# Optimization experiments

Measured on AMD Instinct MI355X. Metric: run time of the kernel, lower is better.

The kernel has to match this reference:

```python
import jax, jax.numpy as jnp
import numpy as np

B, S, E = 2, 2048, 1024
H = 16
HD = E // H           # 64
KD = 64               # k_dim
VD = 64               # v_dim
SCALE = 1.0 / np.float32(np.sqrt(KD))


def setup_inputs() -> dict:
    key = jax.random.key(0)
    ks = jax.random.split(key, 10)
    return {
        "x": jax.random.normal(ks[0], (B, S, E), dtype=jnp.float32),
        "mask": jax.random.uniform(ks[1], (S, S), dtype=jnp.float32),
        "Wq": jax.random.normal(ks[2], (HD, KD), dtype=jnp.float32) * 0.05,
        "bq": jax.random.normal(ks[3], (KD,), dtype=jnp.float32) * 0.05,
        "Wk": jax.random.normal(ks[4], (HD, KD), dtype=jnp.float32) * 0.05,
        "bk": jax.random.normal(ks[5], (KD,), dtype=jnp.float32) * 0.05,
        "Wv": jax.random.normal(ks[6], (HD, VD), dtype=jnp.float32) * 0.05,
        "bv": jax.random.normal(ks[7], (VD,), dtype=jnp.float32) * 0.05,
        "Wo": jax.random.normal(ks[8], (H * VD, E), dtype=jnp.float32) * 0.05,
        "bo": jax.random.normal(ks[9], (E,), dtype=jnp.float32) * 0.05,
    }


def reference(x, mask, Wq, bq, Wk, bk, Wv, bv, Wo, bo):
    b, s, e = x.shape
    # (B, S, E) -> (B, H, S, head_dim)
    xh = x.reshape(b, s, H, HD).transpose(0, 2, 1, 3)
    q = jnp.einsum('bhsd,dk->bhsk', xh, Wq) + bq   # (B,H,S,KD)
    k = jnp.einsum('bhsd,dk->bhsk', xh, Wk) + bk   # (B,H,S,KD)
    v = jnp.einsum('bhsd,dv->bhsv', xh, Wv) + bv   # (B,H,S,VD)
    sim = jnp.einsum('bhqk,bhsk->bhqs', q, k) * SCALE  # (B,H,S,S)
    sim = sim * mask[None, None, :, :]                  # multiplicative mask
    attn = jax.nn.softmax(sim, axis=-1)
    out = jnp.einsum('bhqs,bhsv->bhqv', attn, v)        # (B,H,S,VD)
    out = out.transpose(0, 2, 1, 3).reshape(b, s, H * VD)
    return out @ Wo + bo
```

## Files before the change

kernel.cpp:

```cpp
#include <hip/hip_runtime.h>
#include <hip/hip_bf16.h>

#define SS 2048
#define EE 1024
#define SCALE 0.125f
#define LOG2E 1.44269504088896f

typedef __attribute__((ext_vector_type(8))) short short8;
typedef __attribute__((ext_vector_type(4))) float float4v;
typedef __attribute__((ext_vector_type(4))) unsigned int uint4v;

__device__ __forceinline__ unsigned short f2bf(float f) {
  unsigned int u = __float_as_uint(f);
  unsigned int lsb = (u >> 16) & 1u;
  u += 0x7fffu + lsb;
  return (unsigned short)(u >> 16);
}
__device__ __forceinline__ unsigned int pk2bf(float a, float b) {
  __hip_bfloat162 h = __float22bfloat162_rn(float2{a, b});
  return *reinterpret_cast<unsigned int*>(&h);
}

__global__ __launch_bounds__(256) void fused_qkv(
    const float* __restrict__ x,
    const float* __restrict__ Wq, const float* __restrict__ Wk,
    const float* __restrict__ Wv,
    const float* __restrict__ bq, const float* __restrict__ bk,
    const float* __restrict__ bv,
    const float* __restrict__ mask, const float* __restrict__ Wo,
    unsigned short* __restrict__ Q, unsigned short* __restrict__ Kp,
    unsigned short* __restrict__ Vf,
    unsigned short* __restrict__ maskP, unsigned short* __restrict__ WoT)
{
  __shared__ __align__(16) unsigned short w3t[192 * 72];
  __shared__ __align__(16) unsigned short xt[64 * 72];
  __shared__ __align__(16) unsigned short ob[12288];
  __shared__ float sBias[192];
  __shared__ unsigned short t[64 * 65];
  int blk = blockIdx.x;
  int tid = threadIdx.x;

  if (blk >= 512) {
    if (blk < 2560) {
      int idx = (blk - 512) * 256 + tid;
      int lane = idx & 63, step = (idx >> 6) & 63, qt = idx >> 12;
      int li = lane & 15, g = lane >> 4;
      const float c = SCALE * LOG2E;
      const float* mrow = mask + (size_t)(qt * 16 + li) * SS + step * 32 + g * 4;
      float4 a = *(const float4*)mrow;
      float4 bb = *(const float4*)(mrow + 16);
      uint4v o;
      o.x = pk2bf(a.x * c, a.y * c);
      o.y = pk2bf(a.z * c, a.w * c);
      o.z = pk2bf(bb.x * c, bb.y * c);
      o.w = pk2bf(bb.z * c, bb.w * c);
      *(uint4v*)(maskP + (size_t)idx * 8) = o;
      return;
    }
    int wblk = blk - 2560;
    int k0 = (wblk >> 4) * 64, n0 = (wblk & 15) * 64;
#pragma unroll
    for (int i = 0; i < 16; ++i) {
      int e = tid + i * 256; int kk = e >> 6, nn = e & 63;
      t[nn * 65 + kk] = f2bf(Wo[(size_t)(k0 + kk) * 1024 + n0 + nn]);
    }
    __syncthreads();
#pragma unroll
    for (int i = 0; i < 16; ++i) {
      int e = tid + i * 256; int nn = e >> 6, kk = e & 63;
      WoT[(size_t)(n0 + nn) * 1024 + k0 + kk] = t[nn * 65 + kk];
    }
    return;
  }

  int bh = blk >> 4;
  int s0blk = (blk & 15) * 128;
  int b = bh >> 4, h = bh & 15;
  int wv = tid >> 6, lane = tid & 63;
  int li = lane & 15, g = lane >> 4;

  {
    const float* Ws[3] = {Wq, Wk, Wv};
#pragma unroll
    for (int m = 0; m < 3; ++m) {
      const float* W = Ws[m];
#pragma unroll
      for (int i = 0; i < 16; ++i) {
        int e = tid + i * 256; int d = e >> 6, n = e & 63;
        w3t[(m * 64 + n) * 72 + d] = f2bf(W[e]);
      }
    }
  }
  if (tid < 192) sBias[tid] = (tid < 64) ? bq[tid] : (tid < 128 ? bk[tid - 64] : bv[tid - 128]);

  for (int half = 0; half < 2; ++half) {
    int s0 = s0blk + half * 64;
    if (half) __syncthreads();
    const float* xbase = x + ((size_t)(b * SS + s0)) * EE + h * 64;
#pragma unroll
    for (int it = 0; it < 4; ++it) {
      int flat = tid + it * 256;
      int row = flat >> 4, ch = flat & 15;
      float4 v = *(const float4*)(xbase + (size_t)row * EE + ch * 4);
      uint2 u; u.x = pk2bf(v.x, v.y); u.y = pk2bf(v.z, v.w);
      *(uint2*)(xt + row * 72 + ch * 4) = u;
    }
    __syncthreads();

    int mrow = wv * 16;
    short8 af[2];
#pragma unroll
    for (int ks = 0; ks < 2; ++ks)
      af[ks] = *(const short8*)(xt + (mrow + li) * 72 + ks * 32 + g * 8);

    float4v acc[12];
#pragma unroll
    for (int i = 0; i < 12; ++i) acc[i] = (float4v){0, 0, 0, 0};
#pragma unroll
    for (int ks = 0; ks < 2; ++ks)
#pragma unroll
      for (int nb = 0; nb < 12; ++nb) {
        short8 bfr = *(const short8*)(w3t + (nb * 16 + li) * 72 + ks * 32 + g * 8);
        acc[nb] = __builtin_amdgcn_mfma_f32_16x16x32_bf16(af[ks], bfr, acc[nb], 0, 0, 0);
      }

#pragma unroll
    for (int nb = 0; nb < 12; ++nb) {
      float bias = sBias[nb * 16 + li];
      int mtx = nb >> 2, sub = nb & 3;
#pragma unroll
      for (int r = 0; r < 4; ++r) {
        unsigned short v = f2bf(acc[nb][r] + bias);
        int sl = mrow + g * 4 + r;
        int stp = sl >> 5, s5 = sl & 31;
        if (mtx == 0) {
          ob[sl * 64 + sub * 16 + li] = v;
        } else if (mtx == 1) {
          int sb = s5 >> 4, lik = s5 & 15;
          int part = sub >> 1;
          int gk = ((sub & 1) << 1) | (li >> 3);
          ob[4096 + stp * 2048 + (sb * 2 + part) * 512 + (gk * 16 + lik) * 8 + (li & 7)] = v;
        } else {
          int pos = ((s5 >> 2) & 3) * 8 + ((s5 >> 4) & 1) * 4 + (s5 & 3);
          ob[8192 + stp * 2048 + sub * 512 + ((pos >> 3) * 16 + li) * 8 + (pos & 7)] = v;
        }
      }
    }
    __syncthreads();

    unsigned short* Qg = Q + ((size_t)bh * SS + s0) * 64;
    unsigned short* Kg = Kp + (size_t)bh * 131072 + (s0 >> 5) * 2048;
    unsigned short* Vg = Vf + (size_t)bh * 131072 + (s0 >> 5) * 2048;
#pragma unroll
    for (int i = 0; i < 6; ++i) {
      int slot = tid + i * 256;
      int rgn = slot >> 9, off = (slot & 511) * 8;
      short8 v = *(const short8*)(ob + rgn * 4096 + off);
      unsigned short* dst = (rgn == 0) ? (Qg + off) : (rgn == 1 ? (Kg + off) : (Vg + off));
      *(short8*)dst = v;
    }
  }
}

__global__ __launch_bounds__(256) void attn_kernel(
    const unsigned short* __restrict__ Q, const unsigned short* __restrict__ Kp,
    const unsigned short* __restrict__ Vf, const unsigned short* __restrict__ maskP,
    unsigned short* __restrict__ AO)
{
  __shared__ __align__(16) unsigned short tr_all[4 * 32 * 72];
  int tid = threadIdx.x, wv = tid >> 6, lane = tid & 63;
  int li = lane & 15, g = lane >> 4;
  int virt = (blockIdx.x & 7) * 64 + (blockIdx.x >> 3);
  int wave_id = virt * 4 + wv;
  int bh = wave_id >> 6;
  int q0 = (wave_id & 63) * 32;

  short8 qf[2][2];
#pragma unroll
  for (int t = 0; t < 2; ++t) {
    const unsigned short* Qb = Q + ((size_t)bh * SS + q0 + t * 16 + li) * 64;
    qf[t][0] = *(const short8*)(Qb + g * 8);
    qf[t][1] = *(const short8*)(Qb + 32 + g * 8);
  }

  const unsigned short* Kg = Kp + (size_t)bh * 131072 + lane * 8;
  const unsigned short* Vg = Vf + (size_t)bh * 131072 + lane * 8;
  const unsigned short* Mg0 = maskP + (size_t)(q0 >> 4) * 32768 + lane * 8;
  const unsigned short* Mg1 = Mg0 + 32768;

  unsigned short ov = (li == 0) ? (unsigned short)0x3F80 : (unsigned short)0;
  short8 vones = {(short)ov, (short)ov, (short)ov, (short)ov,
                  (short)ov, (short)ov, (short)ov, (short)ov};

  float4v acc[2][4];
#pragma unroll
  for (int t = 0; t < 2; ++t)
#pragma unroll
    for (int nb = 0; nb < 4; ++nb) acc[t][nb] = (float4v){0, 0, 0, 0};
  float4v accd[2] = {{0, 0, 0, 0}, {0, 0, 0, 0}};

  float4v st[2][2];

  short8 kA[4], kB[4], vA[4], vB[4];
  uint4v mA0, mA1, mB0, mB1;
  {
    short8 k0[4];
#pragma unroll
    for (int i = 0; i < 4; ++i) {
      k0[i] = *(const short8*)(Kg + i * 512);
      kA[i] = *(const short8*)(Kg + 2048 + i * 512);
      kB[i] = *(const short8*)(Kg + 2 * 2048 + i * 512);
      vA[i] = *(const short8*)(Vg + i * 512);
      vB[i] = *(const short8*)(Vg + 2048 + i * 512);
    }
    mA0 = *(const uint4v*)Mg0;
    mA1 = *(const uint4v*)Mg1;
    mB0 = *(const uint4v*)(Mg0 + 512);
    mB1 = *(const uint4v*)(Mg1 + 512);
#pragma unroll
    for (int t = 0; t < 2; ++t)
#pragma unroll
      for (int sb = 0; sb < 2; ++sb) {
        float4v s = {0, 0, 0, 0};
        s = __builtin_amdgcn_mfma_f32_16x16x32_bf16(k0[sb * 2], qf[t][0], s, 0, 0, 0);
        s = __builtin_amdgcn_mfma_f32_16x16x32_bf16(k0[sb * 2 + 1], qf[t][1], s, 0, 0, 0);
        st[t][sb] = s;
      }
  }

  const unsigned short* kpA = Kg + 3 * 2048;
  const unsigned short* kpB = Kg + 4 * 2048;
  const unsigned short* vpA = Vg + 2 * 2048;
  const unsigned short* vpB = Vg + 3 * 2048;
  const unsigned short* mp0 = Mg0 + 2 * 512;
  const unsigned short* mp1 = Mg1 + 2 * 512;

  auto half_step = [&](short8 (&kf)[4], short8 (&vf)[4], uint4v& m0c, uint4v& m1c,
                       const unsigned short* kre, const unsigned short* vre,
                       const unsigned short* mre0, const unsigned short* mre1) {
    short8 pf[2];
#pragma unroll
    for (int t = 0; t < 2; ++t) {
      uint4v pw2;
#pragma unroll
      for (int sb = 0; sb < 2; ++sb) {
#pragma unroll
        for (int hh = 0; hh < 2; ++hh) {
          unsigned int mm = (t == 0) ? m0c[sb * 2 + hh] : m1c[sb * 2 + hh];
          float p0 = __builtin_amdgcn_exp2f(st[t][sb][2 * hh] * __uint_as_float(mm << 16));
          float p1 = __builtin_amdgcn_exp2f(st[t][sb][2 * hh + 1] * __uint_as_float(mm & 0xffff0000u));
          pw2[sb * 2 + hh] = pk2bf(p0, p1);
        }
      }
      pf[t] = *(short8*)&pw2;
    }
    m0c = *(const uint4v*)mre0;
    m1c = *(const uint4v*)mre1;
    __builtin_amdgcn_s_setprio(1);
#pragma unroll
    for (int t = 0; t < 2; ++t)
#pragma unroll
      for (int sb = 0; sb < 2; ++sb) {
        float4v s = {0, 0, 0, 0};
        s = __builtin_amdgcn_mfma_f32_16x16x32_bf16(kf[sb * 2], qf[t][0], s, 0, 0, 0);
        s = __builtin_amdgcn_mfma_f32_16x16x32_bf16(kf[sb * 2 + 1], qf[t][1], s, 0, 0, 0);
        st[t][sb] = s;
      }
    __builtin_amdgcn_s_setprio(0);
#pragma unroll
    for (int i = 0; i < 4; ++i)
      kf[i] = *(const short8*)(kre + i * 512);
    __builtin_amdgcn_s_setprio(1);
#pragma unroll
    for (int nb = 0; nb < 4; ++nb) {
      acc[0][nb] = __builtin_amdgcn_mfma_f32_16x16x32_bf16(vf[nb], pf[0], acc[0][nb], 0, 0, 0);
      acc[1][nb] = __builtin_amdgcn_mfma_f32_16x16x32_bf16(vf[nb], pf[1], acc[1][nb], 0, 0, 0);
    }
    accd[0] = __builtin_amdgcn_mfma_f32_16x16x32_bf16(vones, pf[0], accd[0], 0, 0, 0);
    accd[1] = __builtin_amdgcn_mfma_f32_16x16x32_bf16(vones, pf[1], accd[1], 0, 0, 0);
    __builtin_amdgcn_s_setprio(0);
#pragma unroll
    for (int i = 0; i < 4; ++i)
      vf[i] = *(const short8*)(vre + i * 512);
  };

#pragma unroll 1
  for (int su = 0; su < 32; ++su) {
    half_step(kA, vA, mA0, mA1, kpA, vpA, mp0, mp1);
    half_step(kB, vB, mB0, mB1, kpB, vpB, mp0 + 512, mp1 + 512);
    kpA += 4096; kpB += 4096; vpA += 4096; vpB += 4096;
    mp0 += 1024; mp1 += 1024;
  }

  unsigned short* tr = tr_all + wv * (32 * 72);
#pragma unroll
  for (int t = 0; t < 2; ++t) {
    float den = __shfl(accd[t][0], li, 64);
    float rd = 1.0f / den;
#pragma unroll
    for (int nb = 0; nb < 4; ++nb) {
      int base = (t * 16 + li) * 72 + nb * 16 + g * 4;
      *(unsigned int*)(tr + base)     = pk2bf(acc[t][nb][0] * rd, acc[t][nb][1] * rd);
      *(unsigned int*)(tr + base + 2) = pk2bf(acc[t][nb][2] * rd, acc[t][nb][3] * rd);
    }
  }
  asm volatile("s_waitcnt lgkmcnt(0)" ::: "memory");

  int b = bh >> 4, h = bh & 15;
  int rrow = lane >> 3, part = lane & 7;
#pragma unroll
  for (int i = 0; i < 4; ++i) {
    int row = i * 8 + rrow;
    short8 o = *(const short8*)(tr + row * 72 + part * 8);
    *(short8*)(AO + ((size_t)(b * SS + q0 + row)) * EE + h * 64 + part * 8) = o;
  }
}

__global__ __launch_bounds__(256) void out_gemm(
    const unsigned short* __restrict__ AO, const unsigned short* __restrict__ WoT,
    const float* __restrict__ bo, float* __restrict__ out)
{
  __shared__ __align__(16) unsigned short at[128 * 72];
  __shared__ __align__(16) unsigned short bt[64 * 72];
  int tid = threadIdx.x, wv = tid >> 6, lane = tid & 63;
  int li = lane & 15, g = lane >> 4;
  int m0 = (blockIdx.x >> 4) * 128;
  int n0 = (blockIdx.x & 15) * 64;
  int wm = (wv & 1) * 64, wn = (wv >> 1) * 32;

  const unsigned short* Ag = AO + (size_t)m0 * 1024;
  const unsigned short* Bg = WoT + (size_t)n0 * 1024;
  int srow = tid >> 3, scol = (tid & 7) * 8;

  short8 apre[4], bpre[2];
  auto ldst = [&](int k0) {
#pragma unroll
    for (int i = 0; i < 4; ++i)
      apre[i] = *(const short8*)(Ag + (size_t)(srow + i * 32) * 1024 + k0 + scol);
#pragma unroll
    for (int i = 0; i < 2; ++i) {
      int slot = tid + i * 256;
      int row = slot >> 3, col = (slot & 7) * 8;
      bpre[i] = *(const short8*)(Bg + (size_t)row * 1024 + k0 + col);
    }
  };

  float4v acc[4][2];
#pragma unroll
  for (int mt = 0; mt < 4; ++mt)
#pragma unroll
    for (int nt = 0; nt < 2; ++nt) acc[mt][nt] = (float4v){0, 0, 0, 0};

  ldst(0);
  for (int k0 = 0; k0 < 1024; k0 += 64) {
    __syncthreads();
#pragma unroll
    for (int i = 0; i < 4; ++i)
      *(short8*)(at + (srow + i * 32) * 72 + scol) = apre[i];
#pragma unroll
    for (int i = 0; i < 2; ++i) {
      int slot = tid + i * 256;
      int row = slot >> 3, col = (slot & 7) * 8;
      *(short8*)(bt + row * 72 + col) = bpre[i];
    }
    int nk = (k0 + 64 < 1024) ? k0 + 64 : 0;
    ldst(nk);
    __syncthreads();
#pragma unroll
    for (int ks = 0; ks < 2; ++ks) {
      short8 afr[4], bfr[2];
#pragma unroll
      for (int mt = 0; mt < 4; ++mt)
        afr[mt] = *(const short8*)(at + (wm + mt * 16 + li) * 72 + ks * 32 + g * 8);
#pragma unroll
      for (int nt = 0; nt < 2; ++nt)
        bfr[nt] = *(const short8*)(bt + (wn + nt * 16 + li) * 72 + ks * 32 + g * 8);
#pragma unroll
      for (int mt = 0; mt < 4; ++mt)
#pragma unroll
        for (int nt = 0; nt < 2; ++nt)
          acc[mt][nt] = __builtin_amdgcn_mfma_f32_16x16x32_bf16(afr[mt], bfr[nt], acc[mt][nt], 0, 0, 0);
    }
  }
#pragma unroll
  for (int nt = 0; nt < 2; ++nt) {
    float bof = bo[n0 + wn + nt * 16 + li];
#pragma unroll
    for (int mt = 0; mt < 4; ++mt)
#pragma unroll
      for (int r = 0; r < 4; ++r)
        out[(size_t)(m0 + wm + mt * 16 + g * 4 + r) * 1024 + n0 + wn + nt * 16 + li] =
            acc[mt][nt][r] + bof;
  }
}

extern "C" void kernel_launch(void* const* d_in, const int* in_sizes, int n_in,
                              void* d_out, int out_size, void* d_ws, size_t ws_size,
                              hipStream_t stream) {
  const float* x    = (const float*)d_in[0];
  const float* mask = (const float*)d_in[1];
  const float* Wq   = (const float*)d_in[2];
  const float* bq   = (const float*)d_in[3];
  const float* Wk   = (const float*)d_in[4];
  const float* bk   = (const float*)d_in[5];
  const float* Wv   = (const float*)d_in[6];
  const float* bv   = (const float*)d_in[7];
  const float* Wo   = (const float*)d_in[8];
  const float* bo   = (const float*)d_in[9];
  float* out = (float*)d_out;

  unsigned short* ws = (unsigned short*)d_ws;
  unsigned short* Q     = ws;
  unsigned short* Kp    = ws + 4194304;
  unsigned short* Vf    = ws + 8388608;
  unsigned short* AO    = ws + 12582912;
  unsigned short* maskP = ws + 16777216;
  unsigned short* WoT   = ws + 20971520;

  fused_qkv<<<2816, 256, 0, stream>>>(x, Wq, Wk, Wv, bq, bk, bv, mask, Wo,
                                      Q, Kp, Vf, maskP, WoT);
  attn_kernel<<<512, 256, 0, stream>>>(Q, Kp, Vf, maskP, AO);
  out_gemm<<<512, 256, 0, stream>>>(AO, WoT, bo, out);
}
```

Measured before the change: 172.1 us.

## Load MFMA fragments directly from global memory in out_gemm, dropping LDS staging

The output projection GEMM no longer stages A and B tiles through shared memory with block barriers. Each wave now loads its MFMA operand fragments straight from global memory into registers, double-buffered two k-steps ahead. This removes LDS writes, LDS reads and syncthreads. In exchange, data shared between waves is no longer reused: each wave re-fetches rows that other waves also read, which raises global/L2 traffic and register use. The global reads are also less coalesced, since each lane reads 16-byte pieces at row strides.

```diff
diff --git a/kernel.cpp b/kernel.cpp
--- a/kernel.cpp
+++ b/kernel.cpp
@@ -320,30 +320,29 @@
     const unsigned short* __restrict__ AO, const unsigned short* __restrict__ WoT,
     const float* __restrict__ bo, float* __restrict__ out)
 {
-  __shared__ __align__(16) unsigned short at[128 * 72];
-  __shared__ __align__(16) unsigned short bt[64 * 72];
   int tid = threadIdx.x, wv = tid >> 6, lane = tid & 63;
   int li = lane & 15, g = lane >> 4;
   int m0 = (blockIdx.x >> 4) * 128;
   int n0 = (blockIdx.x & 15) * 64;
   int wm = (wv & 1) * 64, wn = (wv >> 1) * 32;
 
-  const unsigned short* Ag = AO + (size_t)m0 * 1024;
-  const unsigned short* Bg = WoT + (size_t)n0 * 1024;
-  int srow = tid >> 3, scol = (tid & 7) * 8;
-
-  short8 apre[4], bpre[2];
-  auto ldst = [&](int k0) {
-#pragma unroll
-    for (int i = 0; i < 4; ++i)
-      apre[i] = *(const short8*)(Ag + (size_t)(srow + i * 32) * 1024 + k0 + scol);
-#pragma unroll
-    for (int i = 0; i < 2; ++i) {
-      int slot = tid + i * 256;
-      int row = slot >> 3, col = (slot & 7) * 8;
-      bpre[i] = *(const short8*)(Bg + (size_t)row * 1024 + k0 + col);
-    }
+  const unsigned short* Abase = AO + (size_t)(m0 + wm + li) * 1024 + g * 8;
+  const unsigned short* Bbase = WoT + (size_t)(n0 + wn + li) * 1024 + g * 8;
+
+  auto ldA = [&](short8 (&A)[4][2], int k0) {
+#pragma unroll
+    for (int mt = 0; mt < 4; ++mt)
+#pragma unroll
+      for (int ks = 0; ks < 2; ++ks)
+        A[mt][ks] = *(const short8*)(Abase + (size_t)mt * 16 * 1024 + k0 + ks * 32);
   };
+  auto ldB = [&](short8 (&Bf)[2][2], int k0) {
+#pragma unroll
+    for (int nt = 0; nt < 2; ++nt)
+#pragma unroll
+      for (int ks = 0; ks < 2; ++ks)
+        Bf[nt][ks] = *(const short8*)(Bbase + (size_t)nt * 16 * 1024 + k0 + ks * 32);
+  };
 
   float4v acc[4][2];
 #pragma unroll
@@ -351,37 +350,32 @@
 #pragma unroll
     for (int nt = 0; nt < 2; ++nt) acc[mt][nt] = (float4v){0, 0, 0, 0};
 
-  ldst(0);
-  for (int k0 = 0; k0 < 1024; k0 += 64) {
-    __syncthreads();
-#pragma unroll
-    for (int i = 0; i < 4; ++i)
-      *(short8*)(at + (srow + i * 32) * 72 + scol) = apre[i];
-#pragma unroll
-    for (int i = 0; i < 2; ++i) {
-      int slot = tid + i * 256;
-      int row = slot >> 3, col = (slot & 7) * 8;
-      *(short8*)(bt + row * 72 + col) = bpre[i];
-    }
-    int nk = (k0 + 64 < 1024) ? k0 + 64 : 0;
-    ldst(nk);
-    __syncthreads();
-#pragma unroll
-    for (int ks = 0; ks < 2; ++ks) {
-      short8 afr[4], bfr[2];
+  auto mma = [&](short8 (&A)[4][2], short8 (&Bf)[2][2]) {
+#pragma unroll
+    for (int ks = 0; ks < 2; ++ks)
 #pragma unroll
       for (int mt = 0; mt < 4; ++mt)
-        afr[mt] = *(const short8*)(at + (wm + mt * 16 + li) * 72 + ks * 32 + g * 8);
-#pragma unroll
-      for (int nt = 0; nt < 2; ++nt)
-        bfr[nt] = *(const short8*)(bt + (wn + nt * 16 + li) * 72 + ks * 32 + g * 8);
-#pragma unroll
-      for (int mt = 0; mt < 4; ++mt)
 #pragma unroll
         for (int nt = 0; nt < 2; ++nt)
-          acc[mt][nt] = __builtin_amdgcn_mfma_f32_16x16x32_bf16(afr[mt], bfr[nt], acc[mt][nt], 0, 0, 0);
-    }
-  }
+          acc[mt][nt] = __builtin_amdgcn_mfma_f32_16x16x32_bf16(A[mt][ks], Bf[nt][ks], acc[mt][nt], 0, 0, 0);
+  };
+
+  short8 A0[4][2], A1[4][2], B0[2][2], B1[2][2];
+  ldA(A0, 0);   ldB(B0, 0);
+  ldA(A1, 64);  ldB(B1, 64);
+
+#pragma unroll 1
+  for (int su = 0; su < 7; ++su) {
+    mma(A0, B0);
+    ldA(A0, su * 128 + 128);
+    ldB(B0, su * 128 + 128);
+    mma(A1, B1);
+    ldA(A1, su * 128 + 192);
+    ldB(B1, su * 128 + 192);
+  }
+  mma(A0, B0);
+  mma(A1, B1);
+
 #pragma unroll
   for (int nt = 0; nt < 2; ++nt) {
     float bof = bo[n0 + wn + nt * 16 + li];
```

After: 198.4 us. 1.15x slower.
